# Optimization experiments

Measured on AMD Instinct MI355X. Metric: run time of the kernel, lower is better.

Reference implementation:

```python
import jax, jax.numpy as jnp
import numpy as np

N, E = 100000, 1600000          # nodes, edges
DIN, DH, DOUT = 256, 128, 1      # input_dim, hidden_dim, output_dim


def _lin_init(k, din, dout):
    # mimic torch Linear init scale (values don't affect correctness testing)
    s = 1.0 / np.sqrt(din)
    kw, kb = jax.random.split(k)
    W = jax.random.uniform(kw, (din, dout), jnp.float32, -s, s)
    b = jax.random.uniform(kb, (dout,), jnp.float32, -s, s)
    return W, b


def setup_inputs() -> dict:
    key = jax.random.key(0)
    ks = jax.random.split(key, 6)
    x = jax.random.normal(ks[0], (N, DIN), dtype=jnp.float32)
    edge_index = jax.random.randint(ks[1], (2, E), 0, N, dtype=jnp.int64 if jax.config.jax_enable_x64 else jnp.int32)
    W1, b1 = _lin_init(ks[2], DIN, DH)
    W2, b2 = _lin_init(ks[3], DH, DH)
    W3, b3 = _lin_init(ks[4], DH, DH // 2)
    Wc, bc = _lin_init(ks[5], DH // 2, DOUT)
    return {"x": x, "edge_index": edge_index,
            "W1": W1, "b1": b1, "W2": W2, "b2": b2,
            "W3": W3, "b3": b3, "Wc": Wc, "bc": bc}


def _gcn_conv(x, W, b, src, dst, norm_e, norm_self):
    # PyG GCNConv: h = X W; out_i = sum_{j->i} norm_ij h_j + norm_ii h_i + b
    h = x @ W                                           # [N, dout]
    msgs = h[src] * norm_e[:, None]                     # [E, dout] gather
    agg = jax.ops.segment_sum(msgs, dst, num_segments=x.shape[0])  # scatter
    return agg + h * norm_self[:, None] + b


def reference(x, edge_index, W1, b1, W2, b2, W3, b3, Wc, bc):
    src, dst = edge_index[0], edge_index[1]
    n = x.shape[0]
    # symmetric GCN normalization with self-loops: deg = in-degree(A) + 1
    deg = jax.ops.segment_sum(jnp.ones(src.shape[0], x.dtype), dst, num_segments=n) + 1.0
    dinv = jax.lax.rsqrt(deg)
    norm_e = dinv[src] * dinv[dst]   # per-edge norm
    norm_self = dinv * dinv          # self-loop norm

    h = jax.nn.relu(_gcn_conv(x, W1, b1, src, dst, norm_e, norm_self))
    # dropout is identity in eval mode
    h = jax.nn.relu(_gcn_conv(h, W2, b2, src, dst, norm_e, norm_self))
    h = jax.nn.relu(_gcn_conv(h, W3, b3, src, dst, norm_e, norm_self))
    return h @ Wc + bc               # [N, 1]
```

## Files before the change

kernel.cpp:

```cpp
#include <hip/hip_runtime.h>
#include <cstdint>
#include <cstddef>

typedef __attribute__((ext_vector_type(4))) float f32x4;
typedef __attribute__((ext_vector_type(8))) _Float16 half8v;
typedef __attribute__((ext_vector_type(2))) _Float16 half2v;

static inline int cdiv(int a, int b){ return (a + b - 1) / b; }

#define BSH 9
#define CH 8192
#define HCH 8192


__global__ __launch_bounds__(256) void wcvt_bhist_kernel(const float* __restrict__ W1, _Float16* __restrict__ W1t,
                                                         const float* __restrict__ W2, _Float16* __restrict__ W2t,
                                                         const float* __restrict__ W3, _Float16* __restrict__ W3t,
                                                         const int* __restrict__ dst, int* __restrict__ bktcnt,
                                                         int E, int NBK){
  __shared__ int hist[1024];
  int b = blockIdx.x, t = threadIdx.x;
  if (b < 224){
    int i = b * 256 + t;
    if (b < 128){
      int k = i / 128, n = i & 127;
      W1t[(size_t)n * 256 + k] = (_Float16)W1[i];
    } else if (b < 192){
      int j = i - 128 * 256;
      int k = j / 128, n = j & 127;
      W2t[(size_t)n * 128 + k] = (_Float16)W2[j];
    } else {
      int j = i - 192 * 256;
      int k = j / 64, n = j & 63;
      W3t[(size_t)n * 128 + k] = (_Float16)W3[j];
    }
    return;
  }
  int cb = b - 224;
  for (int i = t; i < NBK; i += 256) hist[i] = 0;
  __syncthreads();
  int e0 = cb * HCH;
  int e1 = e0 + HCH; if (e1 > E) e1 = E;
  for (int i = e0 + t; i < e1; i += 256){
    int d = __builtin_nontemporal_load(dst + i);
    atomicAdd(&hist[d >> BSH], 1);
  }
  __syncthreads();
  for (int i = t; i < NBK; i += 256){
    int h = hist[i];
    if (h) atomicAdd(&bktcnt[i], h);
  }
}


__global__ __launch_bounds__(256) void bucket_scan_kernel(const int* __restrict__ bktcnt, int* __restrict__ bbase,
                                                          int* __restrict__ bcur, int NBK, int E){
  __shared__ int sdata[256];
  int t = threadIdx.x;
  int c = (t < NBK) ? bktcnt[t] : 0;
  sdata[t] = c;
  __syncthreads();
  for (int off = 1; off < 256; off <<= 1){
    int v = (t >= off) ? sdata[t - off] : 0;
    __syncthreads();
    sdata[t] += v;
    __syncthreads();
  }
  if (t < NBK){
    int ex = sdata[t] - c;
    bbase[t] = ex;
    bcur[t] = ex;
  }
  if (t == 0) bbase[NBK] = E;
}


__global__ __launch_bounds__(256) void bucket_scatter_kernel(const int* __restrict__ src, const int* __restrict__ dst,
                                                             int* __restrict__ bcur, unsigned* __restrict__ tmp,
                                                             int E, int NBK){
  __shared__ int hist[1024];
  __shared__ int hbase[1024];
  __shared__ unsigned pk[CH];
  __shared__ unsigned short bkt[CH];
  int t = threadIdx.x;
  int e0 = blockIdx.x * CH;
  int e1 = e0 + CH; if (e1 > E) e1 = E;
  int nloc = e1 - e0;
  for (int i = t; i < NBK; i += 256) hist[i] = 0;
  __syncthreads();
  for (int i = t; i < nloc; i += 256){
    int d = __builtin_nontemporal_load(dst + e0 + i);
    int s = __builtin_nontemporal_load(src + e0 + i);
    int b = d >> BSH;
    pk[i]  = ((unsigned)s << BSH) | (unsigned)(d & ((1 << BSH) - 1));
    bkt[i] = (unsigned short)b;
    atomicAdd(&hist[b], 1);
  }
  __syncthreads();
  for (int i = t; i < NBK; i += 256){
    int h = hist[i];
    hbase[i] = h ? atomicAdd(&bcur[i], h) : 0;
    hist[i] = 0;
  }
  __syncthreads();
  for (int i = t; i < nloc; i += 256){
    int b = bkt[i];
    int pos = atomicAdd(&hist[b], 1);
    tmp[hbase[b] + pos] = pk[i];
  }
}


__global__ __launch_bounds__(256) void bucket_build_kernel(const unsigned* __restrict__ tmp, const int* __restrict__ bbase,
                                                           int* __restrict__ row_off, float* __restrict__ dinv,
                                                           int* __restrict__ csr_src, int N, int E, int NBK){
  __shared__ int hist[512];
  __shared__ int sdata[256];
  __shared__ int lofs[512];
  int g = blockIdx.x;
  int base = g << BSH;
  int nloc = N - base; if (nloc > 512) nloc = 512;
  int t = threadIdx.x;
  int rs = bbase[g], re = bbase[g + 1];
  hist[t] = 0; hist[t + 256] = 0;
  __syncthreads();
  for (int i = rs + t; i < re; i += 256)
    atomicAdd(&hist[tmp[i] & 511], 1);
  __syncthreads();
  int h0 = hist[2 * t], h1 = hist[2 * t + 1];
  int pairsum = h0 + h1;
  sdata[t] = pairsum;
  __syncthreads();
  for (int off = 1; off < 256; off <<= 1){
    int v = (t >= off) ? sdata[t - off] : 0;
    __syncthreads();
    sdata[t] += v;
    __syncthreads();
  }
  int ex = sdata[t] - pairsum;
  lofs[2 * t] = ex;
  lofs[2 * t + 1] = ex + h0;
  __syncthreads();
  for (int j = t; j < nloc; j += 256){
    dinv[base + j] = rsqrtf((float)hist[j] + 1.0f);
    row_off[base + j] = rs + lofs[j];
  }
  if (g == NBK - 1 && t == 0) row_off[N] = E;
  __syncthreads();
  for (int j = t; j < 512; j += 256) hist[j] = rs + lofs[j];
  __syncthreads();
  for (int i = rs + t; i < re; i += 256){
    unsigned v = tmp[i];
    int slot = atomicAdd(&hist[v & 511], 1);
    csr_src[slot] = (int)(v >> BSH);
  }
}


template<int BN, bool A32IN>
__global__ __launch_bounds__(256) void mgemm_kernel(const void* __restrict__ Ain, const _Float16* __restrict__ Bt,
                                                    _Float16* __restrict__ C16, const float* __restrict__ dscale,
                                                    int M, int K){
  constexpr int BM = 128, LD = 40;
  constexpr int MF = (BN == 128) ? 4 : 2;
  constexpr int NBC = (BN * 4) / 256;
  __shared__ _Float16 As[BM * LD];
  __shared__ _Float16 Bs[BN * LD];
  const float*    A32 = (const float*)Ain;
  const _Float16* A16 = (const _Float16*)Ain;
  int t = threadIdx.x;
  int w = t >> 6, l = t & 63;
  int m0 = blockIdx.x * BM;
  int wm = (BN == 128) ? (w >> 1) * 64 : w * 32;
  int wn = (BN == 128) ? (w & 1) * 64 : 0;
  int lr = l & 15;
  int kg = (l >> 4) * 8;

  int arow = t >> 2, ac = t & 3;
  int ag0 = m0 + arow, ag1 = m0 + arow + 64;

  f32x4 acc[MF][4];
  #pragma unroll
  for (int i = 0; i < MF; i++)
    #pragma unroll
    for (int j = 0; j < 4; j++){
      f32x4 z = {0.f, 0.f, 0.f, 0.f};
      acc[i][j] = z;
    }

  float4 ar0[2][2];
  half8v ar16[2];
  half8v br[NBC];

  auto loadA = [&](int k0){
    if (A32IN){
      #pragma unroll
      for (int j = 0; j < 2; j++){
        int gr = (j == 0) ? ag0 : ag1;
        if (gr < M){
          const float* ap = A32 + (size_t)gr * K + k0 + ac * 8;
          ar0[j][0] = *reinterpret_cast<const float4*>(ap);
          ar0[j][1] = *reinterpret_cast<const float4*>(ap + 4);
        } else {
          ar0[j][0] = make_float4(0.f, 0.f, 0.f, 0.f);
          ar0[j][1] = make_float4(0.f, 0.f, 0.f, 0.f);
        }
      }
    } else {
      #pragma unroll
      for (int j = 0; j < 2; j++){
        int gr = (j == 0) ? ag0 : ag1;
        if (gr < M){
          ar16[j] = *reinterpret_cast<const half8v*>(A16 + (size_t)gr * K + k0 + ac * 8);
        } else {
          half8v z = {(_Float16)0, (_Float16)0, (_Float16)0, (_Float16)0,
                      (_Float16)0, (_Float16)0, (_Float16)0, (_Float16)0};
          ar16[j] = z;
        }
      }
    }
  };
  auto loadB = [&](int k0){
    #pragma unroll
    for (int j = 0; j < NBC; j++){
      int i = t + j * 256;
      int row = i >> 2, c = i & 3;
      br[j] = *reinterpret_cast<const half8v*>(Bt + (size_t)row * K + k0 + c * 8);
    }
  };
  auto storeLDS = [&](){
    #pragma unroll
    for (int j = 0; j < 2; j++){
      int row = arow + j * 64;
      half8v hv;
      if (A32IN){
        hv[0] = (_Float16)ar0[j][0].x; hv[1] = (_Float16)ar0[j][0].y;
        hv[2] = (_Float16)ar0[j][0].z; hv[3] = (_Float16)ar0[j][0].w;
        hv[4] = (_Float16)ar0[j][1].x; hv[5] = (_Float16)ar0[j][1].y;
        hv[6] = (_Float16)ar0[j][1].z; hv[7] = (_Float16)ar0[j][1].w;
      } else {
        hv = ar16[j];
      }
      *reinterpret_cast<half8v*>(&As[row * LD + ac * 8]) = hv;
    }
    #pragma unroll
    for (int j = 0; j < NBC; j++){
      int i = t + j * 256;
      int row = i >> 2, c = i & 3;
      *reinterpret_cast<half8v*>(&Bs[row * LD + c * 8]) = br[j];
    }
  };

  loadA(0); loadB(0);
  for (int k0 = 0; k0 < K; k0 += 32){
    storeLDS();
    __syncthreads();
    if (k0 + 32 < K){ loadA(k0 + 32); loadB(k0 + 32); }
    half8v af[MF];
    #pragma unroll
    for (int mf = 0; mf < MF; mf++)
      af[mf] = *reinterpret_cast<const half8v*>(&As[(wm + mf * 16 + lr) * LD + kg]);
    #pragma unroll
    for (int nf = 0; nf < 4; nf++){
      half8v bf = *reinterpret_cast<const half8v*>(&Bs[(wn + nf * 16 + lr) * LD + kg]);
      #pragma unroll
      for (int mf = 0; mf < MF; mf++)
        acc[mf][nf] = __builtin_amdgcn_mfma_f32_16x16x32_f16(af[mf], bf, acc[mf][nf], 0, 0, 0);
    }
    __syncthreads();
  }
  #pragma unroll
  for (int mf = 0; mf < MF; mf++){
    #pragma unroll
    for (int r = 0; r < 4; r++){
      int row = m0 + wm + mf * 16 + (l >> 4) * 4 + r;
      if (row < M){
        float sc = dscale[row];
        #pragma unroll
        for (int nf = 0; nf < 4; nf++)
          C16[(size_t)row * BN + wn + nf * 16 + lr] = (_Float16)(sc * acc[mf][nf][r]);
      }
    }
  }
}


__global__ __launch_bounds__(256) void agg128h_kernel(const _Float16* __restrict__ h16, const int* __restrict__ row_off,
                                                      const int* __restrict__ csr_src, const float* __restrict__ dinv,
                                                      const float* __restrict__ bias, _Float16* __restrict__ out16, int n){
  int node = blockIdx.x * 4 + (threadIdx.x >> 6);
  if (node >= n) return;
  int lane = threadIdx.x & 63;
  int e = row_off[node], eend = row_off[node + 1];
  float di = dinv[node];
  half2v sv = *reinterpret_cast<const half2v*>(h16 + (size_t)node * 128 + lane * 2);
  float ax = (float)sv[0], ay = (float)sv[1];
  while (e < eend){
    int m = eend - e; if (m > 64) m = 64;
    int idx = (lane < m) ? csr_src[e + lane] : 0;
    int i = 0;
    for (; i + 16 <= m; i += 16){
      half2v v[16];
      #pragma unroll
      for (int j = 0; j < 16; j++){
        int s = __shfl(idx, i + j);
        v[j] = *reinterpret_cast<const half2v*>(h16 + (size_t)s * 128 + lane * 2);
      }
      #pragma unroll
      for (int j = 0; j < 16; j++){ ax += (float)v[j][0]; ay += (float)v[j][1]; }
    }
    for (; i + 4 <= m; i += 4){
      half2v v[4];
      #pragma unroll
      for (int j = 0; j < 4; j++){
        int s = __shfl(idx, i + j);
        v[j] = *reinterpret_cast<const half2v*>(h16 + (size_t)s * 128 + lane * 2);
      }
      #pragma unroll
      for (int j = 0; j < 4; j++){ ax += (float)v[j][0]; ay += (float)v[j][1]; }
    }
    for (; i < m; i++){
      int s = __shfl(idx, i);
      half2v v = *reinterpret_cast<const half2v*>(h16 + (size_t)s * 128 + lane * 2);
      ax += (float)v[0]; ay += (float)v[1];
    }
    e += m;
  }
  float2 bv = *reinterpret_cast<const float2*>(bias + lane * 2);
  float ox = fmaxf(fmaf(di, ax, bv.x), 0.f);
  float oy = fmaxf(fmaf(di, ay, bv.y), 0.f);
  half2v o; o[0] = (_Float16)ox; o[1] = (_Float16)oy;
  *reinterpret_cast<half2v*>(out16 + (size_t)node * 128 + lane * 2) = o;
}


__global__ __launch_bounds__(256) void agg64h_cls_kernel(const _Float16* __restrict__ h16, const int* __restrict__ row_off,
                                                         const int* __restrict__ csr_src, const float* __restrict__ dinv,
                                                         const float* __restrict__ bias, const float* __restrict__ Wc,
                                                         const float* __restrict__ bc, float* __restrict__ out, int n){
  int node = blockIdx.x * 4 + (threadIdx.x >> 6);
  if (node >= n) return;
  int lane = threadIdx.x & 63;
  int e = row_off[node], eend = row_off[node + 1];
  float di = dinv[node];
  float a = (float)h16[(size_t)node * 64 + lane];
  while (e < eend){
    int m = eend - e; if (m > 64) m = 64;
    int idx = (lane < m) ? csr_src[e + lane] : 0;
    int i = 0;
    for (; i + 16 <= m; i += 16){
      _Float16 v[16];
      #pragma unroll
      for (int j = 0; j < 16; j++){
        int s = __shfl(idx, i + j);
        v[j] = h16[(size_t)s * 64 + lane];
      }
      #pragma unroll
      for (int j = 0; j < 16; j++) a += (float)v[j];
    }
    for (; i + 4 <= m; i += 4){
      _Float16 v[4];
      #pragma unroll
      for (int j = 0; j < 4; j++){
        int s = __shfl(idx, i + j);
        v[j] = h16[(size_t)s * 64 + lane];
      }
      #pragma unroll
      for (int j = 0; j < 4; j++) a += (float)v[j];
    }
    for (; i < m; i++){
      int s = __shfl(idx, i);
      a += (float)h16[(size_t)s * 64 + lane];
    }
    e += m;
  }
  float o = fmaxf(fmaf(di, a, bias[lane]), 0.f);
  float v = o * Wc[lane];
  #pragma unroll
  for (int off = 32; off > 0; off >>= 1) v += __shfl_down(v, off);
  if (lane == 0) out[node] = v + bc[0];
}


extern "C" void kernel_launch(void* const* d_in, const int* in_sizes, int n_in,
                              void* d_out, int out_size, void* d_ws, size_t ws_size,
                              hipStream_t stream){
  const float* x  = (const float*)d_in[0];
  const int*   ei = (const int*)d_in[1];
  const float* W1 = (const float*)d_in[2];
  const float* b1 = (const float*)d_in[3];
  const float* W2 = (const float*)d_in[4];
  const float* b2 = (const float*)d_in[5];
  const float* W3 = (const float*)d_in[6];
  const float* b3 = (const float*)d_in[7];
  const float* Wc = (const float*)d_in[8];
  const float* bc = (const float*)d_in[9];
  float* out = (float*)d_out;

  int N = in_sizes[0] / 256;
  int E = in_sizes[1] / 2;
  const int* src = ei;
  const int* dst = ei + E;
  int NBK = (N + (1 << BSH) - 1) >> BSH;

  char* ws = (char*)d_ws;
  size_t off = 0;
  auto alloc = [&](size_t bytes) -> char* {
    char* p = ws + off;
    off += (bytes + 511) & ~(size_t)511;
    return p;
  };
  int*      bktcnt  = (int*)     alloc((size_t)NBK * 4);
  int*      bbase   = (int*)     alloc(((size_t)NBK + 1) * 4);
  int*      bcur    = (int*)     alloc((size_t)NBK * 4);
  float*    dinv    = (float*)   alloc((size_t)N * 4);
  int*      row_off = (int*)     alloc(((size_t)N + 1) * 4);
  unsigned* tmp     = (unsigned*)alloc((size_t)E * 4);
  int*      csr_src = (int*)     alloc((size_t)E * 4);
  _Float16* bufH    = (_Float16*)alloc((size_t)N * 128 * 2);
  _Float16* bufG    = (_Float16*)alloc((size_t)N * 128 * 2);
  _Float16* W1t     = (_Float16*)alloc((size_t)256 * 128 * 2);
  _Float16* W2t     = (_Float16*)alloc((size_t)128 * 128 * 2);
  _Float16* W3t     = (_Float16*)alloc((size_t)128 * 64 * 2);

  hipMemsetAsync(bktcnt, 0, (size_t)NBK * 4, stream);
  wcvt_bhist_kernel<<<224 + cdiv(E, HCH), 256, 0, stream>>>(W1, W1t, W2, W2t, W3, W3t, dst, bktcnt, E, NBK);
  bucket_scan_kernel<<<1, 256, 0, stream>>>(bktcnt, bbase, bcur, NBK, E);
  bucket_scatter_kernel<<<cdiv(E, CH), 256, 0, stream>>>(src, dst, bcur, tmp, E, NBK);
  bucket_build_kernel<<<NBK, 256, 0, stream>>>(tmp, bbase, row_off, dinv, csr_src, N, E, NBK);
  mgemm_kernel<128, true ><<<cdiv(N, 128), 256, 0, stream>>>(x, W1t, bufH, dinv, N, 256);
  agg128h_kernel<<<cdiv(N, 4), 256, 0, stream>>>(bufH, row_off, csr_src, dinv, b1, bufG, N);
  mgemm_kernel<128, false><<<cdiv(N, 128), 256, 0, stream>>>(bufG, W2t, bufH, dinv, N, 128);
  agg128h_kernel<<<cdiv(N, 4), 256, 0, stream>>>(bufH, row_off, csr_src, dinv, b2, bufG, N);
  mgemm_kernel<64, false><<<cdiv(N, 128), 256, 0, stream>>>(bufG, W3t, bufH, dinv, N, 128);
  agg64h_cls_kernel<<<cdiv(N, 4), 256, 0, stream>>>(bufH, row_off, csr_src, dinv, b3, Wc, bc, out, N);
}
```

Before: 304.6 us.

## Fuse neighbor aggregation with following layer GEMM via shared-memory tile

Result: slower. 393.5 us (+29.2%).

```diff
diff --git a/kernel.cpp b/kernel.cpp
--- a/kernel.cpp
+++ b/kernel.cpp
@@ -285,52 +285,104 @@
 }
 
 
-__global__ __launch_bounds__(256) void agg128h_kernel(const _Float16* __restrict__ h16, const int* __restrict__ row_off,
-                                                      const int* __restrict__ csr_src, const float* __restrict__ dinv,
-                                                      const float* __restrict__ bias, _Float16* __restrict__ out16, int n){
-  int node = blockIdx.x * 4 + (threadIdx.x >> 6);
-  if (node >= n) return;
-  int lane = threadIdx.x & 63;
-  int e = row_off[node], eend = row_off[node + 1];
-  float di = dinv[node];
-  half2v sv = *reinterpret_cast<const half2v*>(h16 + (size_t)node * 128 + lane * 2);
-  float ax = (float)sv[0], ay = (float)sv[1];
-  while (e < eend){
-    int m = eend - e; if (m > 64) m = 64;
-    int idx = (lane < m) ? csr_src[e + lane] : 0;
-    int i = 0;
-    for (; i + 16 <= m; i += 16){
-      half2v v[16];
-      #pragma unroll
-      for (int j = 0; j < 16; j++){
-        int s = __shfl(idx, i + j);
-        v[j] = *reinterpret_cast<const half2v*>(h16 + (size_t)s * 128 + lane * 2);
-      }
-      #pragma unroll
-      for (int j = 0; j < 16; j++){ ax += (float)v[j][0]; ay += (float)v[j][1]; }
-    }
-    for (; i + 4 <= m; i += 4){
-      half2v v[4];
-      #pragma unroll
-      for (int j = 0; j < 4; j++){
-        int s = __shfl(idx, i + j);
-        v[j] = *reinterpret_cast<const half2v*>(h16 + (size_t)s * 128 + lane * 2);
-      }
-      #pragma unroll
-      for (int j = 0; j < 4; j++){ ax += (float)v[j][0]; ay += (float)v[j][1]; }
-    }
-    for (; i < m; i++){
-      int s = __shfl(idx, i);
-      half2v v = *reinterpret_cast<const half2v*>(h16 + (size_t)s * 128 + lane * 2);
-      ax += (float)v[0]; ay += (float)v[1];
-    }
-    e += m;
-  }
-  float2 bv = *reinterpret_cast<const float2*>(bias + lane * 2);
-  float ox = fmaxf(fmaf(di, ax, bv.x), 0.f);
-  float oy = fmaxf(fmaf(di, ay, bv.y), 0.f);
-  half2v o; o[0] = (_Float16)ox; o[1] = (_Float16)oy;
-  *reinterpret_cast<half2v*>(out16 + (size_t)node * 128 + lane * 2) = o;
+template<int BNO>
+__global__ __launch_bounds__(256) void agg_gemm_kernel(const _Float16* __restrict__ h16, const int* __restrict__ row_off,
+                                                       const int* __restrict__ csr_src, const float* __restrict__ dinv,
+                                                       const float* __restrict__ bias, const _Float16* __restrict__ Wt,
+                                                       _Float16* __restrict__ outH, int n){
+  constexpr int ALD = 136;
+  __shared__ _Float16 As[128 * ALD];
+  int t = threadIdx.x, w = t >> 6, l = t & 63;
+  int base = blockIdx.x * 128;
+
+  float2 bv = *reinterpret_cast<const float2*>(bias + l * 2);
+  for (int i = 0; i < 32; i++){
+    int r = w * 32 + i;
+    int nd = base + r;
+    half2v g; g[0] = (_Float16)0; g[1] = (_Float16)0;
+    if (nd < n){
+      int e = row_off[nd], eend = row_off[nd + 1];
+      float di = dinv[nd];
+      half2v sv = *reinterpret_cast<const half2v*>(h16 + (size_t)nd * 128 + l * 2);
+      float ax = (float)sv[0], ay = (float)sv[1];
+      while (e < eend){
+        int m = eend - e; if (m > 64) m = 64;
+        int idx = (l < m) ? csr_src[e + l] : 0;
+        int j = 0;
+        for (; j + 16 <= m; j += 16){
+          half2v v[16];
+          #pragma unroll
+          for (int q = 0; q < 16; q++){
+            int s = __shfl(idx, j + q);
+            v[q] = *reinterpret_cast<const half2v*>(h16 + (size_t)s * 128 + l * 2);
+          }
+          #pragma unroll
+          for (int q = 0; q < 16; q++){ ax += (float)v[q][0]; ay += (float)v[q][1]; }
+        }
+        for (; j + 4 <= m; j += 4){
+          half2v v[4];
+          #pragma unroll
+          for (int q = 0; q < 4; q++){
+            int s = __shfl(idx, j + q);
+            v[q] = *reinterpret_cast<const half2v*>(h16 + (size_t)s * 128 + l * 2);
+          }
+          #pragma unroll
+          for (int q = 0; q < 4; q++){ ax += (float)v[q][0]; ay += (float)v[q][1]; }
+        }
+        for (; j < m; j++){
+          int s = __shfl(idx, j);
+          half2v v = *reinterpret_cast<const half2v*>(h16 + (size_t)s * 128 + l * 2);
+          ax += (float)v[0]; ay += (float)v[1];
+        }
+        e += m;
+      }
+      g[0] = (_Float16)fmaxf(fmaf(di, ax, bv.x), 0.f);
+      g[1] = (_Float16)fmaxf(fmaf(di, ay, bv.y), 0.f);
+    }
+    *reinterpret_cast<half2v*>(&As[r * ALD + l * 2]) = g;
+  }
+  __syncthreads();
+
+  constexpr int MF = (BNO == 128) ? 4 : 2;
+  int wm = (BNO == 128) ? (w >> 1) * 64 : w * 32;
+  int wn = (BNO == 128) ? (w & 1) * 64 : 0;
+  int lr = l & 15;
+  int kg = (l >> 4) * 8;
+  f32x4 acc[MF][4];
+  #pragma unroll
+  for (int i = 0; i < MF; i++)
+    #pragma unroll
+    for (int j = 0; j < 4; j++){
+      f32x4 z = {0.f, 0.f, 0.f, 0.f};
+      acc[i][j] = z;
+    }
+  #pragma unroll
+  for (int kc = 0; kc < 4; kc++){
+    half8v af[MF];
+    #pragma unroll
+    for (int mf = 0; mf < MF; mf++)
+      af[mf] = *reinterpret_cast<const half8v*>(&As[(wm + mf * 16 + lr) * ALD + kc * 32 + kg]);
+    #pragma unroll
+    for (int nf = 0; nf < 4; nf++){
+      half8v bf = *reinterpret_cast<const half8v*>(Wt + (size_t)(wn + nf * 16 + lr) * 128 + kc * 32 + kg);
+      #pragma unroll
+      for (int mf = 0; mf < MF; mf++)
+        acc[mf][nf] = __builtin_amdgcn_mfma_f32_16x16x32_f16(af[mf], bf, acc[mf][nf], 0, 0, 0);
+    }
+  }
+  #pragma unroll
+  for (int mf = 0; mf < MF; mf++){
+    #pragma unroll
+    for (int r = 0; r < 4; r++){
+      int row = base + wm + mf * 16 + (l >> 4) * 4 + r;
+      if (row < n){
+        float sc = dinv[row];
+        #pragma unroll
+        for (int nf = 0; nf < 4; nf++)
+          outH[(size_t)row * BNO + wn + nf * 16 + lr] = (_Float16)(sc * acc[mf][nf][r]);
+      }
+    }
+  }
 }
 
 
@@ -417,8 +469,8 @@
   int*      row_off = (int*)     alloc(((size_t)N + 1) * 4);
   unsigned* tmp     = (unsigned*)alloc((size_t)E * 4);
   int*      csr_src = (int*)     alloc((size_t)E * 4);
-  _Float16* bufH    = (_Float16*)alloc((size_t)N * 128 * 2);
-  _Float16* bufG    = (_Float16*)alloc((size_t)N * 128 * 2);
+  _Float16* bufA    = (_Float16*)alloc((size_t)N * 128 * 2);
+  _Float16* bufB    = (_Float16*)alloc((size_t)N * 128 * 2);
   _Float16* W1t     = (_Float16*)alloc((size_t)256 * 128 * 2);
   _Float16* W2t     = (_Float16*)alloc((size_t)128 * 128 * 2);
   _Float16* W3t     = (_Float16*)alloc((size_t)128 * 64 * 2);
@@ -428,10 +480,8 @@
   bucket_scan_kernel<<<1, 256, 0, stream>>>(bktcnt, bbase, bcur, NBK, E);
   bucket_scatter_kernel<<<cdiv(E, CH), 256, 0, stream>>>(src, dst, bcur, tmp, E, NBK);
   bucket_build_kernel<<<NBK, 256, 0, stream>>>(tmp, bbase, row_off, dinv, csr_src, N, E, NBK);
-  mgemm_kernel<128, true ><<<cdiv(N, 128), 256, 0, stream>>>(x, W1t, bufH, dinv, N, 256);
-  agg128h_kernel<<<cdiv(N, 4), 256, 0, stream>>>(bufH, row_off, csr_src, dinv, b1, bufG, N);
-  mgemm_kernel<128, false><<<cdiv(N, 128), 256, 0, stream>>>(bufG, W2t, bufH, dinv, N, 128);
-  agg128h_kernel<<<cdiv(N, 4), 256, 0, stream>>>(bufH, row_off, csr_src, dinv, b2, bufG, N);
-  mgemm_kernel<64, false><<<cdiv(N, 128), 256, 0, stream>>>(bufG, W3t, bufH, dinv, N, 128);
-  agg64h_cls_kernel<<<cdiv(N, 4), 256, 0, stream>>>(bufH, row_off, csr_src, dinv, b3, Wc, bc, out, N);
-}
+  mgemm_kernel<128, true><<<cdiv(N, 128), 256, 0, stream>>>(x, W1t, bufA, dinv, N, 256);
+  agg_gemm_kernel<128><<<cdiv(N, 128), 256, 0, stream>>>(bufA, row_off, csr_src, dinv, b1, W2t, bufB, N);
+  agg_gemm_kernel<64><<<cdiv(N, 128), 256, 0, stream>>>(bufB, row_off, csr_src, dinv, b2, W3t, bufA, N);
+  agg64h_cls_kernel<<<cdiv(N, 4), 256, 0, stream>>>(bufA, row_off, csr_src, dinv, b3, Wc, bc, out, N);
+}
```
